# Optimization experiments

Hardware: AMD Instinct MI355X
Metric: run time of the kernel (lower is better)

The kernel has to match this reference:

```python
import jax, jax.numpy as jnp
import numpy as np

C_IN = 144
PC = 288           # proj_channels = 2 * in_channels
HEADS = 12
DG = 12            # deformable groups
CLIP = 2
KH = KW = 3
A = KH * KW        # samples per clip per group (attention window 3x3)
PAD = 1
MAXMAG = 10.0
B, T, H, W = 1, 1, 64, 64


def _conv2d(x, w, b, pad):
    y = jax.lax.conv_general_dilated(x, w, (1, 1), [(pad, pad), (pad, pad)],
                                     dimension_numbers=('NCHW', 'OIHW', 'NCHW'))
    return y + b[None, :, None, None]


def _lrelu(x):
    return jnp.where(x >= 0, x, 0.1 * x)


def _linear_c(x, w, b):
    # per-pixel linear on channel dim; x: (..., Cin, h, w), w: (Cin, Cout)
    return jnp.einsum('...ihw,io->...ohw', x, w) + b[:, None, None]


def _bilinear_gather(feat, py, px):
    # feat: (b, clip, g, cg, h, w); py/px: (b, clip, g, A, h, w) absolute pixel coords
    # zero padding outside image (deformable-conv sampling semantics)
    b, cl, g, cg, h, w = feat.shape
    ff = feat.reshape(b, cl, g, cg, h * w)
    y0 = jnp.floor(py)
    x0 = jnp.floor(px)
    wy1 = py - y0
    wx1 = px - x0

    def corner(yc, xc, wt):
        valid = ((yc >= 0) & (yc < h) & (xc >= 0) & (xc < w)).astype(feat.dtype)
        yi = jnp.clip(yc, 0, h - 1).astype(jnp.int32)
        xi = jnp.clip(xc, 0, w - 1).astype(jnp.int32)
        idx = (yi * w + xi).reshape(b, cl, g, 1, -1)
        gat = jnp.take_along_axis(ff, idx, axis=-1).reshape(b, cl, g, cg, *py.shape[3:])
        return gat * (wt * valid)[:, :, :, None]

    out = corner(y0, x0, (1 - wy1) * (1 - wx1))
    out = out + corner(y0, x0 + 1, (1 - wy1) * wx1)
    out = out + corner(y0 + 1, x0, wy1 * (1 - wx1))
    out = out + corner(y0 + 1, x0 + 1, wy1 * wx1)
    return out  # (b, clip, g, cg, A, h, w)


def setup_inputs() -> dict:
    key = jax.random.key(0)
    ks = jax.random.split(key, 32)
    rn = lambda i, shp, s=1.0: jax.random.normal(ks[i], shp, dtype=jnp.float32) * s
    cin_off = C_IN * (1 + CLIP) + CLIP * 2   # 436
    c_off = CLIP * DG * A * 2                # 432
    d = {
        'q': rn(0, (B, T, C_IN, H, W)),
        'k': rn(1, (B, CLIP, C_IN, H, W)),
        'v': rn(2, (B, CLIP, C_IN, H, W)),
        'vpw0': rn(3, (B, T, C_IN, H, W)),
        'vpw1': rn(4, (B, T, C_IN, H, W)),
        'flow0': rn(5, (B, T, 2, H, W), 3.0),
        'flow1': rn(6, (B, T, 2, H, W), 3.0),
        'wo1': rn(7, (64, cin_off, 1, 1), 1.0 / np.sqrt(cin_off)),
        'bo1': rn(8, (64,), 0.01),
        'wo2': rn(9, (64, 64, 3, 3), 1.0 / np.sqrt(64 * 9)),
        'bo2': rn(10, (64,), 0.01),
        'wo3': rn(11, (64, 64, 3, 3), 1.0 / np.sqrt(64 * 9)),
        'bo3': rn(12, (64,), 0.01),
        'wo4': rn(13, (64, 64, 3, 3), 1.0 / np.sqrt(64 * 9)),
        'bo4': rn(14, (64,), 0.01),
        'wo5': rn(15, (64, 64, 3, 3), 1.0 / np.sqrt(64 * 9)),
        'bo5': rn(16, (64,), 0.01),
        'wo6': rn(17, (c_off, 64, 1, 1), 0.02),
        'bo6': rn(18, (c_off,), 0.01),
        'wq': rn(19, (C_IN, PC), 1.0 / np.sqrt(C_IN)),
        'bq': rn(20, (PC,), 0.01),
        'wk': rn(21, (C_IN, PC), 1.0 / np.sqrt(C_IN)),
        'bk': rn(22, (PC,), 0.01),
        'wv': rn(23, (C_IN, PC), 1.0 / np.sqrt(C_IN)),
        'bv': rn(24, (PC,), 0.01),
        'wp': rn(25, (PC, C_IN), 1.0 / np.sqrt(PC)),
        'bp': rn(26, (C_IN,), 0.01),
        'wm1': rn(27, (C_IN, 2 * C_IN), 1.0 / np.sqrt(C_IN)),
        'bm1': rn(28, (2 * C_IN,), 0.01),
        'wm2': rn(29, (2 * C_IN, C_IN), 1.0 / np.sqrt(2 * C_IN)),
        'bm2': rn(30, (C_IN,), 0.01),
    }
    return d


def reference(q, k, v, vpw0, vpw1, flow0, flow1,
              wo1, bo1, wo2, bo2, wo3, bo3, wo4, bo4, wo5, bo5, wo6, bo6,
              wq, bq, wk, bk, wv, bv, wp, bp, wm1, bm1, wm2, bm2):
    b, t, c, h, w = q.shape  # t == 1 here so q batch b*t matches kv batch b
    bt = b * t
    # --- offset predictor: Conv3d stack with time-kernel 1 == 2D convs ---
    x = jnp.concatenate([q, vpw0, vpw1, flow0, flow1], axis=2).reshape(bt, -1, h, w)
    x = _lrelu(_conv2d(x, wo1, bo1, 0))
    x = _lrelu(_conv2d(x, wo2, bo2, 1))
    x = _lrelu(_conv2d(x, wo3, bo3, 1))
    x = _lrelu(_conv2d(x, wo4, bo4, 1))
    x = _lrelu(_conv2d(x, wo5, bo5, 1))
    off = MAXMAG * jnp.tanh(_conv2d(x, wo6, bo6, 0))  # (bt, CLIP*DG*A*2, h, w)
    # add optical flow (channel-flipped to (y, x)) to every sample offset
    fyx = flow0.reshape(bt, 2, h, w)[:, ::-1]
    off = off + jnp.tile(fyx, (1, off.shape[1] // 2, 1, 1))
    off = off.reshape(bt, CLIP, DG, A, 2, h, w)
    ar = jnp.arange(A)
    by = (ar // KW - PAD).astype(q.dtype)  # kernel base offsets (stride=1, dil=1)
    bx = (ar % KW - PAD).astype(q.dtype)
    py = off[:, :, :, :, 0] + by[None, None, None, :, None, None] \
         + jnp.arange(h, dtype=q.dtype)[:, None]
    px = off[:, :, :, :, 1] + bx[None, None, None, :, None, None] \
         + jnp.arange(w, dtype=q.dtype)
    # --- q/k/v projections ---
    hd = PC // HEADS
    qp = _linear_c(q, wq, bq).reshape(bt, HEADS, hd, h, w)
    kp = _linear_c(k, wk, bk).reshape(b, CLIP, DG, PC // DG, h, w)
    vp = _linear_c(v, wv, bv).reshape(b, CLIP, DG, PC // DG, h, w)
    # --- deformable bilinear gather (per deformable group) ---
    ksamp = _bilinear_gather(kp, py, px).reshape(bt, CLIP, HEADS, hd, A, h, w)
    vsamp = _bilinear_gather(vp, py, px).reshape(bt, CLIP, HEADS, hd, A, h, w)
    # --- attention over CLIP*A sampled locations, per pixel per head ---
    scores = jnp.einsum('bmdyx,bcmdayx->bmcayx', qp, ksamp) * (hd ** -0.5)
    attn = jax.nn.softmax(scores.reshape(bt, HEADS, CLIP * A, h, w), axis=2)
    vflat = vsamp.transpose(0, 2, 1, 4, 3, 5, 6).reshape(bt, HEADS, CLIP * A, hd, h, w)
    out = jnp.einsum('bmsyx,bmsdyx->bmdyx', attn, vflat).reshape(b, t, PC, h, w)
    # --- output projection + MLP residual ---
    o = _linear_c(out, wp, bp)
    m = _linear_c(jax.nn.gelu(_linear_c(o, wm1, bm1), approximate=False), wm2, bm2)
    return o + m
```

## Files before the change

### kernel.cpp

```cpp
#include <hip/hip_runtime.h>
#include <hip/hip_bf16.h>
#include <math.h>

typedef __hip_bfloat16 bf16;
typedef __attribute__((ext_vector_type(8))) short bf16x8v;
typedef __attribute__((ext_vector_type(4))) float f32x4v;

#define NPIX 4096

__device__ __forceinline__ float b2f(bf16 v) { return __bfloat162float(v); }
__device__ __forceinline__ unsigned short f2bu(float f) {
    bf16 h = __float2bfloat16(f);
    return *(unsigned short*)&h;
}
__device__ __forceinline__ int detect_bf16(const unsigned short* __restrict__ qraw) {
    int lane = threadIdx.x & 63;
    unsigned short u = qraw[lane * 2];
    int e = (u >> 7) & 0xFF;
    unsigned long long ball = __ballot(e >= 100 && e <= 135);
    return __popcll(ball) > 32;
}
__device__ __forceinline__ float rdval(const void* s, int idx, int isbf) {
    return isbf ? b2f(((const bf16*)s)[idx]) : ((const float*)s)[idx];
}

#define OF_WO6 175680
#define OF_BO6 203328
#define OF_BO1 27904
#define OF_BO2 64832
#define OF_BO3 101760
#define OF_BO4 138688
#define OF_BO5 175616
#define OF_BQ  245232
#define OF_BK  286992
#define OF_BV  328752
#define OF_BP  370512
#define OF_BM1 412128
#define OF_BM2 453888
#define OF_FL0 454032

struct CArgs { const void* src[26]; int dstoff[26]; int n[26]; };
struct PPJob { const void* src; int dstS; int Mp, Kp, kr, mr, sstride, kind; };
struct PPArgs { PPJob j[11]; };

__global__ void misc_kernel(CArgs a, PPArgs pa, const void* __restrict__ q,
                            const void* __restrict__ k, const void* __restrict__ v,
                            const void* __restrict__ vp0, const void* __restrict__ vp1,
                            const void* __restrict__ fl0, const void* __restrict__ fl1,
                            float* __restrict__ cw, short* __restrict__ XS,
                            short* __restrict__ X1, short* __restrict__ wsS)
{
    const int isbf = detect_bf16((const unsigned short*)q);
    const int y = blockIdx.y;
    if (y < 26) {
        const int n = a.n[y];
        float* d = cw + a.dstoff[y];
        if (isbf) {
            const bf16* s = (const bf16*)a.src[y];
            for (int i = blockIdx.x * 256 + threadIdx.x; i < n; i += 256 * 16) d[i] = b2f(s[i]);
        } else {
            const float* s = (const float*)a.src[y];
            for (int i = blockIdx.x * 256 + threadIdx.x; i < n; i += 256 * 16) d[i] = s[i];
        }
    } else if (y < 36) {
        const int job = y - 26;
        const int z = job >> 1, half = job & 1;
        const int p = blockIdx.x * 256 + threadIdx.x;
        const void* srcs[5] = { q, k, k, v, v };
        const int clips[5] = { 0, 0, 1, 0, 1 };
        const size_t co = (size_t)clips[z] * 144 * NPIX;
        short* row = XS + (size_t)z * 655360 + (size_t)p * 160;
        for (int c0 = half * 72; c0 < half * 72 + 72; c0 += 8) {
            unsigned short h[8];
            if (isbf) {
                const bf16* s = (const bf16*)srcs[z] + co;
#pragma unroll
                for (int i = 0; i < 8; ++i) h[i] = f2bu(b2f(s[(size_t)(c0 + i) * NPIX + p]));
            } else {
                const float* s = (const float*)srcs[z] + co;
#pragma unroll
                for (int i = 0; i < 8; ++i) h[i] = f2bu(s[(size_t)(c0 + i) * NPIX + p]);
            }
            uint4 u;
            u.x = (unsigned)h[0] | ((unsigned)h[1] << 16);
            u.y = (unsigned)h[2] | ((unsigned)h[3] << 16);
            u.z = (unsigned)h[4] | ((unsigned)h[5] << 16);
            u.w = (unsigned)h[6] | ((unsigned)h[7] << 16);
            *(uint4*)(row + c0) = u;
        }
        if (half == 1) {
            uint4 zz; zz.x = zz.y = zz.z = zz.w = 0u;
            *(uint4*)(row + 144) = zz;
            *(uint4*)(row + 152) = zz;
        }
    } else if (y < 40) {
        const int sec = y - 36;
        const int p = blockIdx.x * 256 + threadIdx.x;
        short* row = X1 + (size_t)p * 448;
        if (sec < 3) {
            const void* srcs[3] = { q, vp0, vp1 };
            const int cbase = sec * 144;
            for (int c0 = 0; c0 < 144; c0 += 8) {
                unsigned short h[8];
                if (isbf) {
                    const bf16* s = (const bf16*)srcs[sec];
#pragma unroll
                    for (int i = 0; i < 8; ++i) h[i] = f2bu(b2f(s[(size_t)(c0 + i) * NPIX + p]));
                } else {
                    const float* s = (const float*)srcs[sec];
#pragma unroll
                    for (int i = 0; i < 8; ++i) h[i] = f2bu(s[(size_t)(c0 + i) * NPIX + p]);
                }
                uint4 u;
                u.x = (unsigned)h[0] | ((unsigned)h[1] << 16);
                u.y = (unsigned)h[2] | ((unsigned)h[3] << 16);
                u.z = (unsigned)h[4] | ((unsigned)h[5] << 16);
                u.w = (unsigned)h[6] | ((unsigned)h[7] << 16);
                *(uint4*)(row + cbase + c0) = u;
            }
        } else {
            unsigned short h[4];
            if (isbf) {
                const bf16* f0 = (const bf16*)fl0;
                const bf16* f1 = (const bf16*)fl1;
                h[0] = f2bu(b2f(f0[p]));
                h[1] = f2bu(b2f(f0[NPIX + p]));
                h[2] = f2bu(b2f(f1[p]));
                h[3] = f2bu(b2f(f1[NPIX + p]));
            } else {
                const float* f0 = (const float*)fl0;
                const float* f1 = (const float*)fl1;
                h[0] = f2bu(f0[p]);
                h[1] = f2bu(f0[NPIX + p]);
                h[2] = f2bu(f1[p]);
                h[3] = f2bu(f1[NPIX + p]);
            }
            uint4 u;
            u.x = (unsigned)h[0] | ((unsigned)h[1] << 16);
            u.y = (unsigned)h[2] | ((unsigned)h[3] << 16);
            u.z = 0u; u.w = 0u;
            *(uint4*)(row + 432) = u;
            uint4 zz; zz.x = zz.y = zz.z = zz.w = 0u;
            *(uint4*)(row + 440) = zz;
        }
    } else {
        PPJob J = pa.j[y - 40];
        const int tot = J.Mp * J.Kp;
        for (int e = blockIdx.x * 256 + threadIdx.x; e < tot; e += 256 * 16) {
            int m = e / J.Kp, kk = e - m * J.Kp;
            float vv = 0.f;
            if (J.kind == 0) { if (kk < J.kr) vv = rdval(J.src, m * J.sstride + kk, isbf); }
            else if (J.kind == 1) { if (kk < J.kr && m < J.mr) vv = rdval(J.src, kk * J.sstride + m, isbf); }
            else { int c = kk & 63, tap = kk >> 6; if (kk < J.kr) vv = rdval(J.src, m * J.sstride + c * 9 + tap, isbf); }
            wsS[J.dstS + e] = (short)f2bu(vv);
        }
    }
}

struct GemmDesc {
    const short* A; const short* B; const float* bias;
    void* dst; void* dst2; const unsigned short* qraw;
    int Mp, Mreal, mode, gofs, nwaves;
};
struct GemmDesc5 { GemmDesc d[5]; };

template <int TM, int TN, int BM, int KP>
__global__ __launch_bounds__(256) void gemm_kernel(GemmDesc5 gd)
{
    const GemmDesc d = gd.d[blockIdx.z];
    const int wid = blockIdx.x * 4 + (threadIdx.x >> 6);
    if (wid >= d.nwaves) return;
    const int lane = threadIdx.x & 63;
    const int tiles_m = d.Mp / (16 * TM);
    const int m0 = (wid % tiles_m) * (16 * TM);
    const int p0 = (wid / tiles_m) * (16 * TN);
    const int ar = lane & 15;
    const int kq = (lane >> 4) * 8;

    f32x4v acc[TM][TN];
#pragma unroll
    for (int i = 0; i < TM; ++i)
#pragma unroll
        for (int j = 0; j < TN; ++j) acc[i][j] = (f32x4v){0.f, 0.f, 0.f, 0.f};

#pragma unroll
    for (int k0 = 0; k0 < KP; k0 += 32) {
        bf16x8v a[TM], b[TN];
#pragma unroll
        for (int i = 0; i < TM; ++i)
            a[i] = *(const bf16x8v*)(d.A + (size_t)(m0 + i * 16 + ar) * KP + k0 + kq);
        if (BM == 0) {
#pragma unroll
            for (int j = 0; j < TN; ++j)
                b[j] = *(const bf16x8v*)(d.B + (size_t)(p0 + j * 16 + ar) * KP + k0 + kq);
        } else {
            const int tap = k0 >> 6;
            const int cc = (k0 & 63) + kq;
            const int dy = tap / 3 - 1, dx = tap % 3 - 1;
#pragma unroll
            for (int j = 0; j < TN; ++j) {
                const int pix = p0 + j * 16 + ar;
                const int yy = (pix >> 6) + dy, xx = (pix & 63) + dx;
                const bool ok = ((unsigned)yy < 64u) & ((unsigned)xx < 64u);
                const int np = min(max(yy, 0), 63) * 64 + min(max(xx, 0), 63);
                bf16x8v bv = *(const bf16x8v*)(d.B + (size_t)np * 64 + cc);
                if (!ok) bv = (bf16x8v)(short)0;
                b[j] = bv;
            }
        }
#pragma unroll
        for (int i = 0; i < TM; ++i)
#pragma unroll
            for (int j = 0; j < TN; ++j)
                acc[i][j] = __builtin_amdgcn_mfma_f32_16x16x32_bf16(a[i], b[j], acc[i][j], 0, 0, 0);
    }

    const int isbf = (d.mode == 5) ? detect_bf16(d.qraw) : 0;
#pragma unroll
    for (int i = 0; i < TM; ++i) {
#pragma unroll
        for (int j = 0; j < TN; ++j) {
            const int pcol = p0 + j * 16 + (lane & 15);
            const int mb = m0 + i * 16 + (lane >> 4) * 4;
            float vv[4];
#pragma unroll
            for (int r = 0; r < 4; ++r) {
                const int m = mb + r;
                vv[r] = acc[i][j][r];
                if (m < d.Mreal) vv[r] += d.bias[m];
            }
            if (d.mode == 0) {
#pragma unroll
                for (int r = 0; r < 4; ++r) vv[r] = (vv[r] >= 0.f) ? vv[r] : 0.1f * vv[r];
                uint2 u;
                u.x = (unsigned)f2bu(vv[0]) | ((unsigned)f2bu(vv[1]) << 16);
                u.y = (unsigned)f2bu(vv[2]) | ((unsigned)f2bu(vv[3]) << 16);
                *(uint2*)((unsigned short*)d.dst + (size_t)pcol * d.Mp + mb) = u;
            } else if (d.mode == 1) {
                const int g = mb / 24 + d.gofs;
                uint2 u;
                u.x = (unsigned)f2bu(vv[0]) | ((unsigned)f2bu(vv[1]) << 16);
                u.y = (unsigned)f2bu(vv[2]) | ((unsigned)f2bu(vv[3]) << 16);
                *(uint2*)((unsigned short*)d.dst + ((size_t)g * NPIX + pcol) * 24 + (mb % 24)) = u;
            } else if (d.mode == 3) {
                uint2 u;
                u.x = (unsigned)f2bu(vv[0]) | ((unsigned)f2bu(vv[1]) << 16);
                u.y = (unsigned)f2bu(vv[2]) | ((unsigned)f2bu(vv[3]) << 16);
                *(uint2*)((unsigned short*)d.dst + (size_t)pcol * 160 + mb) = u;
                if (mb < 144)
                    *(float4*)((float*)d.dst2 + (size_t)pcol * 144 + mb) =
                        make_float4(vv[0], vv[1], vv[2], vv[3]);
            } else if (d.mode == 4) {
#pragma unroll
                for (int r = 0; r < 4; ++r)
                    vv[r] = 0.5f * vv[r] * (1.f + erff(vv[r] * 0.70710678118654752f));
                uint2 u;
                u.x = (unsigned)f2bu(vv[0]) | ((unsigned)f2bu(vv[1]) << 16);
                u.y = (unsigned)f2bu(vv[2]) | ((unsigned)f2bu(vv[3]) << 16);
                *(uint2*)((unsigned short*)d.dst + (size_t)pcol * d.Mp + mb) = u;
            } else {
#pragma unroll
                for (int r = 0; r < 4; ++r) {
                    const int m = mb + r;
                    if (m < 144) {
                        float v = vv[r] + ((float*)d.dst2)[(size_t)pcol * 144 + m];
                        if (isbf) ((unsigned short*)d.dst)[(size_t)m * NPIX + pcol] = f2bu(v);
                        else      ((float*)d.dst)[(size_t)m * NPIX + pcol] = v;
                    }
                }
            }
        }
    }
}

__global__ __launch_bounds__(256) void conv6_kernel(const short* __restrict__ YF,
                                                    const float* __restrict__ cw,
                                                    float* __restrict__ py, float* __restrict__ px)
{
    const int p = blockIdx.x * 256 + threadIdx.x;
    const int o0 = blockIdx.y * 16;
    const uint4* yrow = (const uint4*)(YF + (size_t)p * 64);
    const float* wb = cw + OF_WO6 + o0 * 64;

    float acc[16];
#pragma unroll
    for (int j = 0; j < 16; ++j) acc[j] = cw[OF_BO6 + o0 + j];

#pragma unroll
    for (int c = 0; c < 8; ++c) {
        uint4 u = yrow[c];
        float a0 = __uint_as_float(u.x << 16);
        float a1 = __uint_as_float(u.x & 0xFFFF0000u);
        float a2 = __uint_as_float(u.y << 16);
        float a3 = __uint_as_float(u.y & 0xFFFF0000u);
        float a4 = __uint_as_float(u.z << 16);
        float a5 = __uint_as_float(u.z & 0xFFFF0000u);
        float a6 = __uint_as_float(u.w << 16);
        float a7 = __uint_as_float(u.w & 0xFFFF0000u);
#pragma unroll
        for (int j = 0; j < 16; ++j) {
            const float* wr = wb + j * 64 + c * 8;
            acc[j] += a0 * wr[0] + a1 * wr[1] + a2 * wr[2] + a3 * wr[3]
                    + a4 * wr[4] + a5 * wr[5] + a6 * wr[6] + a7 * wr[7];
        }
    }

    const float f_y = cw[OF_FL0 + NPIX + p];
    const float f_x = cw[OF_FL0 + p];
    const float yf = (float)(p >> 6), xf = (float)(p & 63);
#pragma unroll
    for (int j = 0; j < 16; ++j) {
        int o = o0 + j;
        float val = 10.f * tanhf(acc[j]);
        int s = o >> 1;
        int a_idx = s % 9;
        if ((o & 1) == 0) py[s * NPIX + p] = val + f_y + (float)(a_idx / 3 - 1) + yf;
        else              px[s * NPIX + p] = val + f_x + (float)(a_idx % 3 - 1) + xf;
    }
}

__device__ __forceinline__ float dot12(const bf16* __restrict__ row, const float* qv) {
    const uint2* s = (const uint2*)row;
    float d = 0.f;
#pragma unroll
    for (int c = 0; c < 3; ++c) {
        uint2 u = s[c];
        d += qv[c * 4 + 0] * __uint_as_float(u.x << 16);
        d += qv[c * 4 + 1] * __uint_as_float(u.x & 0xFFFF0000u);
        d += qv[c * 4 + 2] * __uint_as_float(u.y << 16);
        d += qv[c * 4 + 3] * __uint_as_float(u.y & 0xFFFF0000u);
    }
    return d;
}
__device__ __forceinline__ void acc12(float* ov, const bf16* __restrict__ row, float f) {
    const uint2* s = (const uint2*)row;
#pragma unroll
    for (int c = 0; c < 3; ++c) {
        uint2 u = s[c];
        ov[c * 4 + 0] += f * __uint_as_float(u.x << 16);
        ov[c * 4 + 1] += f * __uint_as_float(u.x & 0xFFFF0000u);
        ov[c * 4 + 2] += f * __uint_as_float(u.y << 16);
        ov[c * 4 + 3] += f * __uint_as_float(u.y & 0xFFFF0000u);
    }
}

__global__ __launch_bounds__(256) void attn_kernel(
    const bf16* __restrict__ qp, const bf16* __restrict__ kp,
    const bf16* __restrict__ vp, const float* __restrict__ py,
    const float* __restrict__ px, unsigned short* __restrict__ att)
{
    const int t = blockIdx.x * 256 + threadIdx.x;
    const int ch = t & 1;
    const int clip = (t >> 1) & 1;
    const int sh = (t >> 2) & 1;
    const int pp = t >> 3;
    const int m = pp >> 12;
    const int p = pp & 4095;

    float qv[12];
    {
        const uint2* s = (const uint2*)(qp + (size_t)(m * 4096 + p) * 24 + ch * 12);
#pragma unroll
        for (int c = 0; c < 3; ++c) {
            uint2 u = s[c];
            qv[c * 4 + 0] = __uint_as_float(u.x << 16);
            qv[c * 4 + 1] = __uint_as_float(u.x & 0xFFFF0000u);
            qv[c * 4 + 2] = __uint_as_float(u.y << 16);
            qv[c * 4 + 3] = __uint_as_float(u.y & 0xFFFF0000u);
        }
    }

    const int gidx = clip * 12 + m;
    const bf16* kb = kp + (size_t)gidx * 4096 * 24 + ch * 12;
    const bf16* vb = vp + (size_t)gidx * 4096 * 24 + ch * 12;
    const int sbase = gidx * 9;
    const int a0 = sh ? 5 : 0;
    const int na = sh ? 4 : 5;

    float e[5], w0s[5], w1s[5], w2s[5], w3s[5];
    int n0s[5], n1s[5], n2s[5], n3s[5];
    float mx = -1e30f;
#pragma unroll
    for (int i = 0; i < 5; ++i) {
        const int a = min(a0 + i, 8);
        const float fy = py[(sbase + a) * NPIX + p];
        const float fx = px[(sbase + a) * NPIX + p];
        const float y0f = floorf(fy), x0f = floorf(fx);
        const float wy = fy - y0f, wx = fx - x0f;
        const int iy = (int)y0f, ix = (int)x0f;
        const float vy0 = ((unsigned)iy < 64u) ? 1.f : 0.f;
        const float vy1 = ((unsigned)(iy + 1) < 64u) ? 1.f : 0.f;
        const float vx0 = ((unsigned)ix < 64u) ? 1.f : 0.f;
        const float vx1 = ((unsigned)(ix + 1) < 64u) ? 1.f : 0.f;
        const int iy0 = min(max(iy, 0), 63), iy1 = min(max(iy + 1, 0), 63);
        const int ix0 = min(max(ix, 0), 63), ix1 = min(max(ix + 1, 0), 63);
        w0s[i] = (1.f - wy) * (1.f - wx) * vy0 * vx0;
        w1s[i] = (1.f - wy) * wx * vy0 * vx1;
        w2s[i] = wy * (1.f - wx) * vy1 * vx0;
        w3s[i] = wy * wx * vy1 * vx1;
        n0s[i] = iy0 * 64 + ix0; n1s[i] = iy0 * 64 + ix1;
        n2s[i] = iy1 * 64 + ix0; n3s[i] = iy1 * 64 + ix1;
        float part = w0s[i] * dot12(kb + (size_t)n0s[i] * 24, qv)
                   + w1s[i] * dot12(kb + (size_t)n1s[i] * 24, qv)
                   + w2s[i] * dot12(kb + (size_t)n2s[i] * 24, qv)
                   + w3s[i] * dot12(kb + (size_t)n3s[i] * 24, qv);
        float full = part + __shfl_xor(part, 1, 64);
        e[i] = (i < na) ? full * 0.20412414523193154f : -1e30f;
        mx = fmaxf(mx, e[i]);
    }
    mx = fmaxf(mx, __shfl_xor(mx, 4, 64));
    mx = fmaxf(mx, __shfl_xor(mx, 2, 64));
    float sum = 0.f;
#pragma unroll
    for (int i = 0; i < 5; ++i) { e[i] = __expf(e[i] - mx); sum += e[i]; }
    sum += __shfl_xor(sum, 4, 64);
    sum += __shfl_xor(sum, 2, 64);
    const float inv = 1.f / sum;

    float ov[12];
#pragma unroll
    for (int j = 0; j < 12; ++j) ov[j] = 0.f;

#pragma unroll
    for (int i = 0; i < 5; ++i) {
        const float wa = e[i] * inv;
        acc12(ov, vb + (size_t)n0s[i] * 24, wa * w0s[i]);
        acc12(ov, vb + (size_t)n1s[i] * 24, wa * w1s[i]);
        acc12(ov, vb + (size_t)n2s[i] * 24, wa * w2s[i]);
        acc12(ov, vb + (size_t)n3s[i] * 24, wa * w3s[i]);
    }
#pragma unroll
    for (int j = 0; j < 12; ++j) {
        ov[j] += __shfl_xor(ov[j], 4, 64);
        ov[j] += __shfl_xor(ov[j], 2, 64);
    }
    if (clip == 0 && sh == 0) {
        unsigned short* ab = att + (size_t)p * 288 + m * 24 + ch * 12;
#pragma unroll
        for (int c = 0; c < 3; ++c) {
            uint2 u;
            u.x = (unsigned)f2bu(ov[c * 4 + 0]) | ((unsigned)f2bu(ov[c * 4 + 1]) << 16);
            u.y = (unsigned)f2bu(ov[c * 4 + 2]) | ((unsigned)f2bu(ov[c * 4 + 3]) << 16);
            ((uint2*)ab)[c] = u;
        }
    }
}

__global__ void diag_kernel(float* __restrict__ out, int n, float v)
{
    int i = blockIdx.x * 256 + threadIdx.x;
    if (i < n) out[i] = (i == 0 ? v : 0.f);
}

extern "C" void kernel_launch(void* const* d_in, const int* in_sizes, int n_in,
                              void* d_out, int out_size, void* d_ws, size_t ws_size,
                              hipStream_t stream)
{
    const size_t REQUIRED = 75000000;
    if (ws_size < REQUIRED) {
        float code = 1000.0f + (float)(ws_size >> 20);
        diag_kernel<<<dim3((out_size + 255) / 256), 256, 0, stream>>>((float*)d_out, out_size, code);
        return;
    }

    char* W = (char*)d_ws;
    short* wsS = (short*)W;
    float* cw = (float*)(W + 64);

    short* conv1w = wsS + 1000000;
    short* conv3w[4] = { wsS + 1028672, wsS + 1065536, wsS + 1102400, wsS + 1139264 };
    short* wqb = wsS + 1176128, *wkb = wsS + 1222208, *wvb = wsS + 1268288;
    short* wpS = wsS + 1314368, *wm1S = wsS + 1360448, *wm2S = wsS + 1406528;

    short* XS = (short*)(W + 16777216);
    short* X1 = (short*)(W + 25165824);
    bf16*  QP = (bf16*)(W + 33554432);
    bf16*  KP = (bf16*)(W + 36700160);
    bf16*  VP = (bf16*)(W + 41943040);
    short* Y0 = (short*)(W + 50331648);
    short* Y1 = (short*)(W + 50855936);
    short* YF = (short*)(W + 51380224);
    float* PY = (float*)(W + 54525952);
    float* PX = (float*)(W + 58064896);
    unsigned short* ATT = (unsigned short*)(W + 62914560);
    short* OPM = (short*)(W + 67108864);
    float* O32 = (float*)(W + 68419584);
    short* M1  = (short*)(W + 71303168);

    const unsigned short* qraw = (const unsigned short*)d_in[0];

    CArgs ca;
    const int srcidx[26] = {7,8,9,10,11,12,13,14,15,16,17,18,19,20,21,22,23,24,25,26,27,28,29,30,5,6};
    const int dsto[26]   = {0,OF_BO1,27968,OF_BO2,64896,OF_BO3,101824,OF_BO4,138752,OF_BO5,
                            OF_WO6,OF_BO6,203760,OF_BQ,245520,OF_BK,287280,OF_BV,329040,OF_BP,
                            370656,OF_BM1,412416,OF_BM2,OF_FL0,462224};
    for (int i = 0; i < 26; ++i) {
        ca.src[i] = d_in[srcidx[i]];
        ca.dstoff[i] = dsto[i];
        ca.n[i] = in_sizes[srcidx[i]];
    }
    PPArgs pp;
    pp.j[0]  = { d_in[7],  1000000, 64, 448, 436, 64,  436, 0 };
    pp.j[1]  = { d_in[9],  1028672, 64, 576, 576, 64,  576, 2 };
    pp.j[2]  = { d_in[11], 1065536, 64, 576, 576, 64,  576, 2 };
    pp.j[3]  = { d_in[13], 1102400, 64, 576, 576, 64,  576, 2 };
    pp.j[4]  = { d_in[15], 1139264, 64, 576, 576, 64,  576, 2 };
    pp.j[5]  = { d_in[19], 1176128, 288, 160, 144, 288, 288, 1 };
    pp.j[6]  = { d_in[21], 1222208, 288, 160, 144, 288, 288, 1 };
    pp.j[7]  = { d_in[23], 1268288, 288, 160, 144, 288, 288, 1 };
    pp.j[8]  = { d_in[25], 1314368, 160, 288, 288, 144, 144, 1 };
    pp.j[9]  = { d_in[27], 1360448, 288, 160, 144, 288, 288, 1 };
    pp.j[10] = { d_in[29], 1406528, 160, 288, 288, 144, 144, 1 };
    misc_kernel<<<dim3(16, 51), 256, 0, stream>>>(ca, pp, d_in[0], d_in[1], d_in[2], d_in[3],
                                                  d_in[4], d_in[5], d_in[6], cw, XS, X1, wsS);

    GemmDesc5 g3;
    const short* Xz[5] = { XS, XS + 655360, XS + 1310720, XS + 1966080, XS + 2621440 };
    const short* Az[5] = { wqb, wkb, wkb, wvb, wvb };
    const float* Bz[5] = { cw + OF_BQ, cw + OF_BK, cw + OF_BK, cw + OF_BV, cw + OF_BV };
    bf16* Dz[5] = { QP, KP, KP, VP, VP };
    const int Gz[5] = { 0, 0, 12, 0, 12 };
    for (int z = 0; z < 5; ++z)
        g3.d[z] = { Az[z], Xz[z], Bz[z], Dz[z], nullptr, qraw, 288, 288, 1, Gz[z], 1152 };
    gemm_kernel<2, 2, 0, 160><<<dim3(288, 1, 5), 256, 0, stream>>>(g3);

    GemmDesc5 g1;
    g1.d[0] = { conv1w, X1, cw + OF_BO1, Y0, nullptr, qraw, 64, 64, 0, 0, 1024 };
    gemm_kernel<1, 1, 0, 448><<<dim3(256, 1, 1), 256, 0, stream>>>(g1);

    const float* cb[4] = { cw + OF_BO2, cw + OF_BO3, cw + OF_BO4, cw + OF_BO5 };
    short* cin[4] = { Y0, Y1, Y0, Y1 };
    short* coutp[4] = { Y1, Y0, Y1, YF };
    for (int i = 0; i < 4; ++i) {
        GemmDesc5 gc;
        gc.d[0] = { conv3w[i], cin[i], cb[i], coutp[i], nullptr, qraw, 64, 64, 0, 0, 1024 };
        gemm_kernel<1, 1, 1, 576><<<dim3(256, 1, 1), 256, 0, stream>>>(gc);
    }

    conv6_kernel<<<dim3(16, 27), 256, 0, stream>>>(YF, cw, PY, PX);

    attn_kernel<<<dim3(1536), 256, 0, stream>>>(QP, KP, VP, PY, PX, ATT);

    GemmDesc5 gwp;
    gwp.d[0] = { wpS, (const short*)ATT, cw + OF_BP, OPM, O32, qraw, 160, 144, 3, 0, 640 };
    gemm_kernel<2, 2, 0, 288><<<dim3(160, 1, 1), 256, 0, stream>>>(gwp);

    GemmDesc5 gm1;
    gm1.d[0] = { wm1S, OPM, cw + OF_BM1, M1, nullptr, qraw, 288, 288, 4, 0, 1152 };
    gemm_kernel<2, 2, 0, 160><<<dim3(288, 1, 1), 256, 0, stream>>>(gm1);

    GemmDesc5 gm2;
    gm2.d[0] = { wm2S, M1, cw + OF_BM2, d_out, O32, qraw, 160, 144, 5, 0, 640 };
    gemm_kernel<2, 2, 0, 288><<<dim3(160, 1, 1), 256, 0, stream>>>(gm2);
}
```

Measured before the change: 279.8 us.

## Use online softmax in deformable attention and drop unused weight copies

The deformable attention kernel now computes the softmax in a single online pass. It keeps a running max and sum, rescales the value accumulator as it goes, and accumulates values in the same loop that gathers keys. This removes the per-sample arrays for weights and indices and the second gather pass, which should lower register pressure, at the cost of extra exp calls and accumulator rescaling. Separately, the misc kernel stops copying 12 fp32 weight tensors that appear to be used only in their packed bf16 form, which shrinks the launch grid.

```diff
diff --git a/kernel.cpp b/kernel.cpp
--- a/kernel.cpp
+++ b/kernel.cpp
@@ -39,7 +39,7 @@
 #define OF_BM2 453888
 #define OF_FL0 454032
 
-struct CArgs { const void* src[26]; int dstoff[26]; int n[26]; };
+struct CArgs { const void* src[14]; int dstoff[14]; int n[14]; };
 struct PPJob { const void* src; int dstS; int Mp, Kp, kr, mr, sstride, kind; };
 struct PPArgs { PPJob j[11]; };
 
@@ -52,7 +52,7 @@
 {
     const int isbf = detect_bf16((const unsigned short*)q);
     const int y = blockIdx.y;
-    if (y < 26) {
+    if (y < 14) {
         const int n = a.n[y];
         float* d = cw + a.dstoff[y];
         if (isbf) {
@@ -62,8 +62,8 @@
             const float* s = (const float*)a.src[y];
             for (int i = blockIdx.x * 256 + threadIdx.x; i < n; i += 256 * 16) d[i] = s[i];
         }
-    } else if (y < 36) {
-        const int job = y - 26;
+    } else if (y < 24) {
+        const int job = y - 14;
         const int z = job >> 1, half = job & 1;
         const int p = blockIdx.x * 256 + threadIdx.x;
         const void* srcs[5] = { q, k, k, v, v };
@@ -93,8 +93,8 @@
             *(uint4*)(row + 144) = zz;
             *(uint4*)(row + 152) = zz;
         }
-    } else if (y < 40) {
-        const int sec = y - 36;
+    } else if (y < 28) {
+        const int sec = y - 24;
         const int p = blockIdx.x * 256 + threadIdx.x;
         short* row = X1 + (size_t)p * 448;
         if (sec < 3) {
@@ -144,7 +144,7 @@
             *(uint4*)(row + 440) = zz;
         }
     } else {
-        PPJob J = pa.j[y - 40];
+        PPJob J = pa.j[y - 28];
         const int tot = J.Mp * J.Kp;
         for (int e = blockIdx.x * 256 + threadIdx.x; e < tot; e += 256 * 16) {
             int m = e / J.Kp, kk = e - m * J.Kp;
@@ -377,62 +377,65 @@
     const int a0 = sh ? 5 : 0;
     const int na = sh ? 4 : 5;
 
-    float e[5], w0s[5], w1s[5], w2s[5], w3s[5];
-    int n0s[5], n1s[5], n2s[5], n3s[5];
-    float mx = -1e30f;
+    float mxL = -1e30f, sumL = 0.f;
+    float ov[12];
+#pragma unroll
+    for (int j = 0; j < 12; ++j) ov[j] = 0.f;
+
 #pragma unroll
     for (int i = 0; i < 5; ++i) {
-        const int a = min(a0 + i, 8);
-        const float fy = py[(sbase + a) * NPIX + p];
-        const float fx = px[(sbase + a) * NPIX + p];
-        const float y0f = floorf(fy), x0f = floorf(fx);
-        const float wy = fy - y0f, wx = fx - x0f;
-        const int iy = (int)y0f, ix = (int)x0f;
-        const float vy0 = ((unsigned)iy < 64u) ? 1.f : 0.f;
-        const float vy1 = ((unsigned)(iy + 1) < 64u) ? 1.f : 0.f;
-        const float vx0 = ((unsigned)ix < 64u) ? 1.f : 0.f;
-        const float vx1 = ((unsigned)(ix + 1) < 64u) ? 1.f : 0.f;
-        const int iy0 = min(max(iy, 0), 63), iy1 = min(max(iy + 1, 0), 63);
-        const int ix0 = min(max(ix, 0), 63), ix1 = min(max(ix + 1, 0), 63);
-        w0s[i] = (1.f - wy) * (1.f - wx) * vy0 * vx0;
-        w1s[i] = (1.f - wy) * wx * vy0 * vx1;
-        w2s[i] = wy * (1.f - wx) * vy1 * vx0;
-        w3s[i] = wy * wx * vy1 * vx1;
-        n0s[i] = iy0 * 64 + ix0; n1s[i] = iy0 * 64 + ix1;
-        n2s[i] = iy1 * 64 + ix0; n3s[i] = iy1 * 64 + ix1;
-        float part = w0s[i] * dot12(kb + (size_t)n0s[i] * 24, qv)
-                   + w1s[i] * dot12(kb + (size_t)n1s[i] * 24, qv)
-                   + w2s[i] * dot12(kb + (size_t)n2s[i] * 24, qv)
-                   + w3s[i] * dot12(kb + (size_t)n3s[i] * 24, qv);
-        float full = part + __shfl_xor(part, 1, 64);
-        e[i] = (i < na) ? full * 0.20412414523193154f : -1e30f;
-        mx = fmaxf(mx, e[i]);
-    }
-    mx = fmaxf(mx, __shfl_xor(mx, 4, 64));
-    mx = fmaxf(mx, __shfl_xor(mx, 2, 64));
-    float sum = 0.f;
-#pragma unroll
-    for (int i = 0; i < 5; ++i) { e[i] = __expf(e[i] - mx); sum += e[i]; }
-    sum += __shfl_xor(sum, 4, 64);
-    sum += __shfl_xor(sum, 2, 64);
-    const float inv = 1.f / sum;
-
-    float ov[12];
-#pragma unroll
-    for (int j = 0; j < 12; ++j) ov[j] = 0.f;
-
-#pragma unroll
-    for (int i = 0; i < 5; ++i) {
-        const float wa = e[i] * inv;
-        acc12(ov, vb + (size_t)n0s[i] * 24, wa * w0s[i]);
-        acc12(ov, vb + (size_t)n1s[i] * 24, wa * w1s[i]);
-        acc12(ov, vb + (size_t)n2s[i] * 24, wa * w2s[i]);
-        acc12(ov, vb + (size_t)n3s[i] * 24, wa * w3s[i]);
-    }
+        if (i < na) {
+            const int a = a0 + i;
+            const float fy = py[(sbase + a) * NPIX + p];
+            const float fx = px[(sbase + a) * NPIX + p];
+            const float y0f = floorf(fy), x0f = floorf(fx);
+            const float wy = fy - y0f, wx = fx - x0f;
+            const int iy = (int)y0f, ix = (int)x0f;
+            const float vy0 = ((unsigned)iy < 64u) ? 1.f : 0.f;
+            const float vy1 = ((unsigned)(iy + 1) < 64u) ? 1.f : 0.f;
+            const float vx0 = ((unsigned)ix < 64u) ? 1.f : 0.f;
+            const float vx1 = ((unsigned)(ix + 1) < 64u) ? 1.f : 0.f;
+            const int iy0 = min(max(iy, 0), 63), iy1 = min(max(iy + 1, 0), 63);
+            const int ix0 = min(max(ix, 0), 63), ix1 = min(max(ix + 1, 0), 63);
+            const float w0 = (1.f - wy) * (1.f - wx) * vy0 * vx0;
+            const float w1 = (1.f - wy) * wx * vy0 * vx1;
+            const float w2 = wy * (1.f - wx) * vy1 * vx0;
+            const float w3 = wy * wx * vy1 * vx1;
+            const int n0 = iy0 * 64 + ix0, n1 = iy0 * 64 + ix1;
+            const int n2 = iy1 * 64 + ix0, n3 = iy1 * 64 + ix1;
+            float part = w0 * dot12(kb + (size_t)n0 * 24, qv)
+                       + w1 * dot12(kb + (size_t)n1 * 24, qv)
+                       + w2 * dot12(kb + (size_t)n2 * 24, qv)
+                       + w3 * dot12(kb + (size_t)n3 * 24, qv);
+            float full = part + __shfl_xor(part, 1, 64);
+            float e = full * 0.20412414523193154f;
+            float newmx = fmaxf(mxL, e);
+            float r = __expf(mxL - newmx);
+            float ee = __expf(e - newmx);
+            mxL = newmx;
+            sumL = sumL * r + ee;
+#pragma unroll
+            for (int j = 0; j < 12; ++j) ov[j] *= r;
+            acc12(ov, vb + (size_t)n0 * 24, ee * w0);
+            acc12(ov, vb + (size_t)n1 * 24, ee * w1);
+            acc12(ov, vb + (size_t)n2 * 24, ee * w2);
+            acc12(ov, vb + (size_t)n3 * 24, ee * w3);
+        }
+    }
+
+    float M = fmaxf(mxL, __shfl_xor(mxL, 4, 64));
+    M = fmaxf(M, __shfl_xor(M, 2, 64));
+    const float sc = __expf(mxL - M);
+    float s = sumL * sc;
+    s += __shfl_xor(s, 4, 64);
+    s += __shfl_xor(s, 2, 64);
+    const float inv = 1.f / s;
 #pragma unroll
     for (int j = 0; j < 12; ++j) {
-        ov[j] += __shfl_xor(ov[j], 4, 64);
-        ov[j] += __shfl_xor(ov[j], 2, 64);
+        float v = ov[j] * sc;
+        v += __shfl_xor(v, 4, 64);
+        v += __shfl_xor(v, 2, 64);
+        ov[j] = v * inv;
     }
     if (clip == 0 && sh == 0) {
         unsigned short* ab = att + (size_t)p * 288 + m * 24 + ch * 12;
@@ -490,11 +493,10 @@
     const unsigned short* qraw = (const unsigned short*)d_in[0];
 
     CArgs ca;
-    const int srcidx[26] = {7,8,9,10,11,12,13,14,15,16,17,18,19,20,21,22,23,24,25,26,27,28,29,30,5,6};
-    const int dsto[26]   = {0,OF_BO1,27968,OF_BO2,64896,OF_BO3,101824,OF_BO4,138752,OF_BO5,
-                            OF_WO6,OF_BO6,203760,OF_BQ,245520,OF_BK,287280,OF_BV,329040,OF_BP,
-                            370656,OF_BM1,412416,OF_BM2,OF_FL0,462224};
-    for (int i = 0; i < 26; ++i) {
+    const int srcidx[14] = {8,10,12,14,16,17,18,20,22,24,26,28,30,5};
+    const int dsto[14]   = {OF_BO1,OF_BO2,OF_BO3,OF_BO4,OF_BO5,OF_WO6,OF_BO6,
+                            OF_BQ,OF_BK,OF_BV,OF_BP,OF_BM1,OF_BM2,OF_FL0};
+    for (int i = 0; i < 14; ++i) {
         ca.src[i] = d_in[srcidx[i]];
         ca.dstoff[i] = dsto[i];
         ca.n[i] = in_sizes[srcidx[i]];
@@ -511,7 +513,7 @@
     pp.j[8]  = { d_in[25], 1314368, 160, 288, 288, 144, 144, 1 };
     pp.j[9]  = { d_in[27], 1360448, 288, 160, 144, 288, 288, 1 };
     pp.j[10] = { d_in[29], 1406528, 160, 288, 288, 144, 144, 1 };
-    misc_kernel<<<dim3(16, 51), 256, 0, stream>>>(ca, pp, d_in[0], d_in[1], d_in[2], d_in[3],
+    misc_kernel<<<dim3(16, 39), 256, 0, stream>>>(ca, pp, d_in[0], d_in[1], d_in[2], d_in[3],
                                                   d_in[4], d_in[5], d_in[6], cw, XS, X1, wsS);
 
     GemmDesc5 g3;
```

Result: slower. 289.2 us (+3.3%).
